# Performance work log

Measured on AMD Instinct MI355X. Metric: run time of the kernel, lower is better.

Reference implementation:

```python
import jax, jax.numpy as jnp
import numpy as np

B, J, D = 1024, 17, 512          # batch, joints, encoder hidden dim
M, K, DT = 34, 2048, 512         # tokens per pose, codebook size, token dim
DDEC, DDEC_I = 32, 64            # decoder hidden dims
L_ENC, L_DEC = 4, 1
DECAY = 0.9
EPS = 1e-5


def _ln(x, g, b):
    m = jnp.mean(x, -1, keepdims=True)
    v = jnp.mean((x - m) ** 2, -1, keepdims=True)
    return (x - m) * jax.lax.rsqrt(v + EPS) * g + b


def _mlp(x, w1, b1, w2, b2):
    return jax.nn.gelu(x @ w1 + b1, approximate=False) @ w2 + b2


def _mixer(x, p, i):
    ln1g, ln1b, tw1, tb1, tw2, tb2, ln2g, ln2b, cw1, cb1, cw2, cb2 = (a[i] for a in p)
    y = jnp.swapaxes(_ln(x, ln1g, ln1b), 1, 2)        # token-mixing over joints
    y = jnp.swapaxes(_mlp(y, tw1, tb1, tw2, tb2), 1, 2)
    z = _mlp(_ln(x + y, ln2g, ln2b), cw1, cb1, cw2, cb2)  # channel-mixing
    return x + y + z


def _forward(joints, invisible_token, start_w, start_b,
             enc_ln1_g, enc_ln1_b, enc_tw1, enc_tb1, enc_tw2, enc_tb2,
             enc_ln2_g, enc_ln2_b, enc_cw1, enc_cb1, enc_cw2, enc_cb2,
             enc_ln_g, enc_ln_b, token_mlp_w, token_mlp_b, feat_w, feat_b,
             dec_ln1_g, dec_ln1_b, dec_tw1, dec_tb1, dec_tw2, dec_tb2,
             dec_ln2_g, dec_ln2_b, dec_cw1, dec_cb1, dec_cw2, dec_cb2,
             dec_token_mlp_w, dec_token_mlp_b, dec_start_w, dec_start_b,
             dec_ln_g, dec_ln_b, rec_w, rec_b,
             codebook, ema_cluster_size, ema_w):
    x = joints[:, :, :2] @ start_w + start_b                  # [B,J,D]
    vis = (joints[:, :, 2:] != 0).astype(x.dtype)             # [B,J,1]
    x = x * vis + invisible_token * (1.0 - vis)
    encp = (enc_ln1_g, enc_ln1_b, enc_tw1, enc_tb1, enc_tw2, enc_tb2,
            enc_ln2_g, enc_ln2_b, enc_cw1, enc_cb1, enc_cw2, enc_cb2)
    for i in range(L_ENC):
        x = _mixer(x, encp, i)
    x = _ln(x, enc_ln_g, enc_ln_b)
    # token_mlp: Linear over joints axis: [B,D,J] -> [B,D,M] -> [B,M,D]
    x = jnp.einsum('bjd,jm->bmd', x, token_mlp_w) + token_mlp_b[None, :, None]
    feat = (x @ feat_w + feat_b).reshape(B * M, DT)           # encode_feat [N,DT]
    # squared euclidean distances to codebook entries
    dists = (jnp.sum(feat * feat, 1, keepdims=True)
             + jnp.sum(codebook * codebook, 1)
             - 2.0 * feat @ codebook.T)                       # [N,K]
    idx = jnp.argmin(dists, axis=1)                           # [N]
    quant = codebook[idx]                                     # == one_hot(idx) @ codebook
    # EMA codebook update (buffers; single-device so all_reduce == identity)
    sg_feat = jax.lax.stop_gradient(feat)
    counts = jax.ops.segment_sum(jnp.ones((B * M,), feat.dtype), idx, num_segments=K)
    dw = jax.ops.segment_sum(sg_feat, idx, num_segments=K)    # == encodings.T @ feat
    cs = ema_cluster_size * DECAY + (1.0 - DECAY) * counts
    n = jnp.sum(cs)
    cs = (cs + 1e-5) / (n + K * 1e-5) * n                     # laplace smoothing
    ema_w_new = ema_w * DECAY + (1.0 - DECAY) * dw
    codebook_new = ema_w_new / cs[:, None]
    e_latent_loss = jnp.mean(jnp.square(jax.lax.stop_gradient(quant) - feat))
    quant = feat + jax.lax.stop_gradient(quant - feat)        # straight-through
    ptf = quant.reshape(B, M, DT)
    out_ptf = jax.lax.stop_gradient(ptf)
    # decoder_token_mlp: Linear over token axis: [B,DT,M] -> [B,DT,J] -> [B,J,DT]
    y = jnp.einsum('bmd,mj->bjd', ptf, dec_token_mlp_w) + dec_token_mlp_b[None, :, None]
    y = y @ dec_start_w + dec_start_b                         # [B,J,DDEC]
    decp = (dec_ln1_g, dec_ln1_b, dec_tw1, dec_tb1, dec_tw2, dec_tb2,
            dec_ln2_g, dec_ln2_b, dec_cw1, dec_cb1, dec_cw2, dec_cb2)
    for i in range(L_DEC):
        y = _mixer(y, decp, i)
    y = _ln(y, dec_ln_g, dec_ln_b)
    rec = y @ rec_w + rec_b                                   # [B,J,2]
    return rec, idx, e_latent_loss, out_ptf, codebook_new


def setup_inputs():
    ks = iter(jax.random.split(jax.random.key(0), 64))
    def nrm(shape, s=0.02):
        return jax.random.normal(next(ks), shape, jnp.float32) * s
    inp = {}
    coords = jax.random.uniform(next(ks), (B, J, 2), jnp.float32)
    inp['joints'] = jnp.concatenate([coords, jnp.ones((B, J, 1), jnp.float32)], -1)
    inp['joints_feature'] = nrm((B, J, 256), 1.0)   # unused (guide_ratio=0)
    inp['cls_logits'] = jnp.zeros((1, 1), jnp.float32)  # unused in tokenizer stage
    inp['invisible_token'] = nrm((1, 1, D))
    inp['start_w'], inp['start_b'] = nrm((2, D)), jnp.zeros((D,), jnp.float32)
    for pre, L, H, HI in (('enc', L_ENC, D, D), ('dec', L_DEC, DDEC, DDEC_I)):
        inp[pre + '_ln1_g'], inp[pre + '_ln1_b'] = jnp.ones((L, H)), jnp.zeros((L, H))
        inp[pre + '_tw1'], inp[pre + '_tb1'] = nrm((L, J, 64)), jnp.zeros((L, 64))
        inp[pre + '_tw2'], inp[pre + '_tb2'] = nrm((L, 64, J)), jnp.zeros((L, J))
        inp[pre + '_ln2_g'], inp[pre + '_ln2_b'] = jnp.ones((L, H)), jnp.zeros((L, H))
        inp[pre + '_cw1'], inp[pre + '_cb1'] = nrm((L, H, HI)), jnp.zeros((L, HI))
        inp[pre + '_cw2'], inp[pre + '_cb2'] = nrm((L, HI, H)), jnp.zeros((L, H))
    inp['enc_ln_g'], inp['enc_ln_b'] = jnp.ones((D,)), jnp.zeros((D,))
    inp['token_mlp_w'], inp['token_mlp_b'] = nrm((J, M)), jnp.zeros((M,))
    inp['feat_w'], inp['feat_b'] = nrm((D, DT)), jnp.zeros((DT,))
    inp['codebook'] = jax.random.normal(next(ks), (K, DT), jnp.float32)
    inp['ema_cluster_size'] = jnp.zeros((K,), jnp.float32)
    inp['ema_w'] = jax.random.normal(next(ks), (K, DT), jnp.float32)
    inp['dec_token_mlp_w'], inp['dec_token_mlp_b'] = nrm((M, J)), jnp.zeros((J,))
    inp['dec_start_w'], inp['dec_start_b'] = nrm((DT, DDEC)), jnp.zeros((DDEC,))
    inp['dec_ln_g'], inp['dec_ln_b'] = jnp.ones((DDEC,)), jnp.zeros((DDEC,))
    inp['rec_w'], inp['rec_b'] = nrm((DDEC, 2)), jnp.zeros((2,))
    return inp


def reference(joints, joints_feature, cls_logits, invisible_token, start_w, start_b,
              enc_ln1_g, enc_ln1_b, enc_tw1, enc_tb1, enc_tw2, enc_tb2,
              enc_ln2_g, enc_ln2_b, enc_cw1, enc_cb1, enc_cw2, enc_cb2,
              enc_ln_g, enc_ln_b, token_mlp_w, token_mlp_b, feat_w, feat_b,
              codebook, ema_cluster_size, ema_w,
              dec_ln1_g, dec_ln1_b, dec_tw1, dec_tb1, dec_tw2, dec_tb2,
              dec_ln2_g, dec_ln2_b, dec_cw1, dec_cb1, dec_cw2, dec_cb2,
              dec_token_mlp_w, dec_token_mlp_b, dec_start_w, dec_start_b,
              dec_ln_g, dec_ln_b, rec_w, rec_b):
    # joints_feature / cls_logits unused: guide_ratio=0, stage_pct='tokenizer'
    return _forward(joints, invisible_token, start_w, start_b,
                    enc_ln1_g, enc_ln1_b, enc_tw1, enc_tb1, enc_tw2, enc_tb2,
                    enc_ln2_g, enc_ln2_b, enc_cw1, enc_cb1, enc_cw2, enc_cb2,
                    enc_ln_g, enc_ln_b, token_mlp_w, token_mlp_b, feat_w, feat_b,
                    dec_ln1_g, dec_ln1_b, dec_tw1, dec_tb1, dec_tw2, dec_tb2,
                    dec_ln2_g, dec_ln2_b, dec_cw1, dec_cb1, dec_cw2, dec_cb2,
                    dec_token_mlp_w, dec_token_mlp_b, dec_start_w, dec_start_b,
                    dec_ln_g, dec_ln_b, rec_w, rec_b,
                    codebook, ema_cluster_size, ema_w)
```

## Files before the change

kernel.cpp:

```cpp
#include <hip/hip_runtime.h>
#include <math.h>

constexpr int Bn = 1024, Jn = 17, Mn = 34;
constexpr int RJ = Bn * Jn;
constexpr int RM = Bn * Mn;
constexpr size_t SZX = (size_t)RJ * 512;
constexpr size_t SZM = (size_t)RM * 512;

typedef __attribute__((ext_vector_type(8))) short bf16x8;
typedef __attribute__((ext_vector_type(4))) float f32x4;
typedef unsigned long long u64;
typedef unsigned short u16;
typedef unsigned int u32;

__device__ __forceinline__ float gelu_f(float x) {
  return 0.5f * x * (1.0f + erff(x * 0.7071067811865475f));
}
__device__ __forceinline__ u16 bf16_rne(float x) {
  u32 u = __float_as_uint(x);
  u += 0x7fffu + ((u >> 16) & 1u);
  return (u16)(u >> 16);
}
__device__ __forceinline__ float bf16_f(u16 h) {
  return __uint_as_float((u32)h << 16);
}

typedef __attribute__((address_space(1))) const void gas_t;
typedef __attribute__((address_space(3))) void las_t;
__device__ __forceinline__ void gll16(const void* g, void* l) {
  __builtin_amdgcn_global_load_lds((gas_t*)g, (las_t*)l, 16, 0, 0);
}

__global__ __launch_bounds__(256) void embed_kernel(
    const float* __restrict__ joints, const float* __restrict__ inv,
    const float* __restrict__ sw, const float* __restrict__ sb,
    float* __restrict__ out) {
  int tid = blockIdx.x * 256 + threadIdx.x;
  int row = tid >> 9, d = tid & 511;
  float j0 = joints[row * 3 + 0];
  float j1 = joints[row * 3 + 1];
  float j2 = joints[row * 3 + 2];
  float x = fmaf(j0, sw[d], fmaf(j1, sw[512 + d], sb[d]));
  float v = (j2 != 0.0f) ? 1.0f : 0.0f;
  out[tid] = x * v + inv[d] * (1.0f - v);
}

__global__ __launch_bounds__(256) void mixer_fused(
    const float* __restrict__ x_in, float* __restrict__ res_out,
    u16* __restrict__ oh, u16* __restrict__ ol,
    const float* __restrict__ g1, const float* __restrict__ b1,
    const float* __restrict__ tw1, const float* __restrict__ tb1,
    const float* __restrict__ tw2, const float* __restrict__ tb2,
    const float* __restrict__ g2, const float* __restrict__ b2) {
  __shared__ float xs[17][512];
  __shared__ float sw1[17 * 64], sw2[64 * 17], sb1v[64], sb2v[17];
  __shared__ float stats[17][2];
  const int tid = threadIdx.x;
  const int b = blockIdx.x;
  for (int i = tid; i < 17 * 64; i += 256) { sw1[i] = tw1[i]; sw2[i] = tw2[i]; }
  if (tid < 64) sb1v[tid] = tb1[tid];
  if (tid < 17) sb2v[tid] = tb2[tid];
  const float* px = x_in + (size_t)b * 17 * 512;
  for (int i = tid; i < 17 * 512; i += 256) xs[i >> 9][i & 511] = px[i];
  __syncthreads();
  const int wv = tid >> 6, ln_ = tid & 63;
  for (int j = wv; j < 17; j += 4) {
    float v[8];
    float s = 0.0f;
#pragma unroll
    for (int i = 0; i < 8; i++) { v[i] = xs[j][ln_ + 64 * i]; s += v[i]; }
#pragma unroll
    for (int m = 32; m; m >>= 1) s += __shfl_xor(s, m);
    float mean = s * (1.0f / 512.0f);
    float s2 = 0.0f;
#pragma unroll
    for (int i = 0; i < 8; i++) { float t = v[i] - mean; s2 += t * t; }
#pragma unroll
    for (int m = 32; m; m >>= 1) s2 += __shfl_xor(s2, m);
    float rs = 1.0f / sqrtf(s2 * (1.0f / 512.0f) + 1e-5f);
    if (ln_ == 0) { stats[j][0] = mean; stats[j][1] = rs; }
  }
  __syncthreads();
  for (int cc = 0; cc < 2; cc++) {
    int d = tid + cc * 256;
    float gd = g1[d], bd = b1[d];
    float t[17], acc[17];
#pragma unroll
    for (int j = 0; j < 17; j++) {
      t[j] = (xs[j][d] - stats[j][0]) * stats[j][1] * gd + bd;
      acc[j] = 0.0f;
    }
    for (int k = 0; k < 64; k++) {
      float h = sb1v[k];
#pragma unroll
      for (int j = 0; j < 17; j++) h = fmaf(t[j], sw1[j * 64 + k], h);
      h = gelu_f(h);
#pragma unroll
      for (int j = 0; j < 17; j++) acc[j] = fmaf(h, sw2[k * 17 + j], acc[j]);
    }
#pragma unroll
    for (int j = 0; j < 17; j++) {
      float r = xs[j][d] + acc[j] + sb2v[j];
      xs[j][d] = r;
      res_out[((size_t)b * 17 + j) * 512 + d] = r;
    }
  }
  __syncthreads();
  for (int j = wv; j < 17; j += 4) {
    float v[8];
    float s = 0.0f;
#pragma unroll
    for (int i = 0; i < 8; i++) { v[i] = xs[j][ln_ + 64 * i]; s += v[i]; }
#pragma unroll
    for (int m = 32; m; m >>= 1) s += __shfl_xor(s, m);
    float mean = s * (1.0f / 512.0f);
    float s2 = 0.0f;
#pragma unroll
    for (int i = 0; i < 8; i++) { float t = v[i] - mean; s2 += t * t; }
#pragma unroll
    for (int m = 32; m; m >>= 1) s2 += __shfl_xor(s2, m);
    float rs = 1.0f / sqrtf(s2 * (1.0f / 512.0f) + 1e-5f);
#pragma unroll
    for (int i = 0; i < 8; i++) {
      int d = ln_ + 64 * i;
      float o = (v[i] - mean) * rs * g2[d] + b2[d];
      u16 h = bf16_rne(o);
      size_t off = ((size_t)b * 17 + j) * 512 + d;
      oh[off] = h;
      ol[off] = bf16_rne(o - bf16_f(h));
    }
  }
}

__global__ __launch_bounds__(256) void lnmix_fused(
    const float* __restrict__ x_in, u16* __restrict__ oh, u16* __restrict__ ol,
    const float* __restrict__ g, const float* __restrict__ bb,
    const float* __restrict__ w, const float* __restrict__ bias) {
  __shared__ float xs[17][513];
  __shared__ float sw[17 * 34], sb[34];
  const int tid = threadIdx.x;
  const int b = blockIdx.x;
  for (int i = tid; i < 17 * 34; i += 256) sw[i] = w[i];
  if (tid < 34) sb[tid] = bias[tid];
  const float* px = x_in + (size_t)b * 17 * 512;
  for (int i = tid; i < 17 * 512; i += 256) xs[i >> 9][i & 511] = px[i];
  __syncthreads();
  const int wv = tid >> 6, ln_ = tid & 63;
  for (int j = wv; j < 17; j += 4) {
    float v[8];
    float s = 0.0f;
#pragma unroll
    for (int i = 0; i < 8; i++) { v[i] = xs[j][ln_ + 64 * i]; s += v[i]; }
#pragma unroll
    for (int m = 32; m; m >>= 1) s += __shfl_xor(s, m);
    float mean = s * (1.0f / 512.0f);
    float s2 = 0.0f;
#pragma unroll
    for (int i = 0; i < 8; i++) { float t = v[i] - mean; s2 += t * t; }
#pragma unroll
    for (int m = 32; m; m >>= 1) s2 += __shfl_xor(s2, m);
    float rs = 1.0f / sqrtf(s2 * (1.0f / 512.0f) + 1e-5f);
#pragma unroll
    for (int i = 0; i < 8; i++) {
      int d = ln_ + 64 * i;
      xs[j][d] = (v[i] - mean) * rs * g[d] + bb[d];
    }
  }
  __syncthreads();
  for (int cc = 0; cc < 2; cc++) {
    int d = tid + cc * 256;
    float t[17];
#pragma unroll
    for (int j = 0; j < 17; j++) t[j] = xs[j][d];
#pragma unroll
    for (int m = 0; m < 34; m++) {
      float s = sb[m];
#pragma unroll
      for (int j = 0; j < 17; j++) s = fmaf(t[j], sw[j * 34 + m], s);
      size_t o = ((size_t)b * 34 + m) * 512 + d;
      u16 h = bf16_rne(s);
      oh[o] = h;
      ol[o] = bf16_rne(s - bf16_f(h));
    }
  }
}

__global__ __launch_bounds__(256) void prep2_wT(
    const float* __restrict__ W1, const float* __restrict__ W2,
    u16* __restrict__ Th1, u16* __restrict__ Tl1,
    u16* __restrict__ Th2, u16* __restrict__ Tl2) {
  int tid = blockIdx.x * 256 + threadIdx.x;
  const float* W = (tid < 262144) ? W1 : W2;
  u16* Th = (tid < 262144) ? Th1 : Th2;
  u16* Tl = (tid < 262144) ? Tl1 : Tl2;
  int t = tid & 262143;
  int k = t >> 9, n = t & 511;
  float v = W[t];
  u16 h = bf16_rne(v);
  Th[(size_t)n * 512 + k] = h;
  Tl[(size_t)n * 512 + k] = bf16_rne(v - bf16_f(h));
}

__global__ __launch_bounds__(256) void prep_wT(
    const float* __restrict__ W, u16* __restrict__ Th, u16* __restrict__ Tl) {
  int tid = blockIdx.x * 256 + threadIdx.x;
  int k = tid >> 9, n = tid & 511;
  float v = W[tid];
  u16 h = bf16_rne(v);
  Th[(size_t)n * 512 + k] = h;
  Tl[(size_t)n * 512 + k] = bf16_rne(v - bf16_f(h));
}

__global__ __launch_bounds__(256) void splitnorm_kernel(
    const float* __restrict__ CBm, u16* __restrict__ hi, u16* __restrict__ lo,
    float* __restrict__ cnorm) {
  int wave = threadIdx.x >> 6, lane = threadIdx.x & 63;
  int k = blockIdx.x * 4 + wave;
  const float4* p4 = (const float4*)(CBm + (size_t)k * 512);
  ushort4* h4 = (ushort4*)(hi + (size_t)k * 512);
  ushort4* l4 = (ushort4*)(lo + (size_t)k * 512);
  float s = 0.0f;
#pragma unroll
  for (int i = 0; i < 2; i++) {
    float4 x = p4[lane + 64 * i];
    ushort4 h, l;
    h.x = bf16_rne(x.x); l.x = bf16_rne(x.x - bf16_f(h.x));
    h.y = bf16_rne(x.y); l.y = bf16_rne(x.y - bf16_f(h.y));
    h.z = bf16_rne(x.z); l.z = bf16_rne(x.z - bf16_f(h.z));
    h.w = bf16_rne(x.w); l.w = bf16_rne(x.w - bf16_f(h.w));
    h4[lane + 64 * i] = h;
    l4[lane + 64 * i] = l;
    s = fmaf(x.x, x.x, s); s = fmaf(x.y, x.y, s);
    s = fmaf(x.z, x.z, s); s = fmaf(x.w, x.w, s);
  }
#pragma unroll
  for (int m = 32; m; m >>= 1) s += __shfl_xor(s, m);
  if (lane == 0) cnorm[k] = s;
}

#define MG_PROLOGUE()                                                        \
  const int tid = threadIdx.x;                                               \
  const int m0 = blockIdx.x * 128, n0 = blockIdx.y * 128;                    \
  const int lane = tid & 63, wave = tid >> 6;                                \
  const int wm = wave >> 1, wn = wave & 1;                                   \
  const int fr = lane & 15, q = lane >> 4, qd = q;                           \
  const int ci0 = wave * 128 + lane, ci1 = ci0 + 64;                         \
  const int r0 = ci0 >> 2, c0x = (ci0 & 3) ^ ((r0 >> 1) & 3);                \
  const int r1 = ci1 >> 2, c1x = (ci1 & 3) ^ ((r1 >> 1) & 3);                \
  const size_t aoff0 = (size_t)(m0 + r0) * 512 + c0x * 8;                    \
  const size_t aoff1 = (size_t)(m0 + r1) * 512 + c1x * 8;                    \
  const size_t boff0 = (size_t)(n0 + r0) * 512 + c0x * 8;                    \
  const size_t boff1 = (size_t)(n0 + r1) * 512 + c1x * 8;                    \
  const int ld0 = wave * 1024, ld1 = ld0 + 512;       \
  int fca[4], fcb[4];                                                        \
  _Pragma("unroll") for (int t4 = 0; t4 < 4; t4++) {                         \
    int rra = wm * 64 + t4 * 16 + fr;                                        \
    int rrb = wn * 64 + t4 * 16 + fr;                                        \
    int sz = q ^ ((fr >> 1) & 3);                                            \
    fca[t4] = (rra * 4 + sz) * 8;                                            \
    fcb[t4] = (rrb * 4 + sz) * 8;                                            \
  }                                                                          \
  f32x4 acc[4][4];                                                           \
  _Pragma("unroll") for (int i = 0; i < 4; i++)                              \
    _Pragma("unroll") for (int j = 0; j < 4; j++) {                          \
      acc[i][j][0] = 0.0f; acc[i][j][1] = 0.0f;                              \
      acc[i][j][2] = 0.0f; acc[i][j][3] = 0.0f;                              \
    }

#define MG_KLOOP(Ah, Al, Bh, Bl)                                             \
  for (int k0 = 0; k0 < 512; k0 += 32) {                                     \
    gll16(Ah + aoff0 + k0, &sAh[ld0]);                                       \
    gll16(Ah + aoff1 + k0, &sAh[ld1]);                                       \
    gll16(Al + aoff0 + k0, &sAl[ld0]);                                       \
    gll16(Al + aoff1 + k0, &sAl[ld1]);                                       \
    gll16(Bh + boff0 + k0, &sBh[ld0]);                                       \
    gll16(Bh + boff1 + k0, &sBh[ld1]);                                       \
    gll16(Bl + boff0 + k0, &sBl[ld0]);                                       \
    gll16(Bl + boff1 + k0, &sBl[ld1]);                                       \
    __syncthreads();                                                         \
    bf16x8 fah[4], fal[4], fbh[4], fbl[4];                                   \
    _Pragma("unroll") for (int t4 = 0; t4 < 4; t4++) {                       \
      fah[t4] = *(const bf16x8*)&sAh[fca[t4]];                               \
      fal[t4] = *(const bf16x8*)&sAl[fca[t4]];                               \
      fbh[t4] = *(const bf16x8*)&sBh[fcb[t4]];                               \
      fbl[t4] = *(const bf16x8*)&sBl[fcb[t4]];                               \
    }                                                                        \
    _Pragma("unroll") for (int mt = 0; mt < 4; mt++)                         \
      _Pragma("unroll") for (int nt = 0; nt < 4; nt++) {                     \
        acc[mt][nt] = __builtin_amdgcn_mfma_f32_16x16x32_bf16(               \
            fah[mt], fbh[nt], acc[mt][nt], 0, 0, 0);                         \
        acc[mt][nt] = __builtin_amdgcn_mfma_f32_16x16x32_bf16(               \
            fah[mt], fbl[nt], acc[mt][nt], 0, 0, 0);                         \
        acc[mt][nt] = __builtin_amdgcn_mfma_f32_16x16x32_bf16(               \
            fal[mt], fbh[nt], acc[mt][nt], 0, 0, 0);                         \
      }                                                                      \
    __syncthreads();                                                         \
  }

template <int GELU_FLAG, int RES_FLAG, int HILO_OUT>
__global__ __launch_bounds__(256, 4) void mgemm(
    const u16* __restrict__ Ah, const u16* __restrict__ Al,
    const u16* __restrict__ Bh, const u16* __restrict__ Bl,
    const float* __restrict__ bias, const float* __restrict__ R,
    float* __restrict__ C, u16* __restrict__ Oh, u16* __restrict__ Ol, int N) {
  __shared__ __align__(16) u16 sAh[4096], sAl[4096], sBh[4096], sBl[4096];
  MG_PROLOGUE()
  MG_KLOOP(Ah, Al, Bh, Bl)
#pragma unroll
  for (int mt = 0; mt < 4; mt++)
#pragma unroll
    for (int reg = 0; reg < 4; reg++) {
      int row = m0 + wm * 64 + mt * 16 + qd * 4 + reg;
#pragma unroll
      for (int nt = 0; nt < 4; nt++) {
        int col = n0 + wn * 64 + nt * 16 + fr;
        float v = acc[mt][nt][reg] + bias[col];
        if (GELU_FLAG) v = gelu_f(v);
        if (RES_FLAG) v += R[(size_t)row * N + col];
        if (HILO_OUT) {
          u16 h = bf16_rne(v);
          Oh[(size_t)row * N + col] = h;
          Ol[(size_t)row * N + col] = bf16_rne(v - bf16_f(h));
        } else {
          C[(size_t)row * N + col] = v;
        }
      }
    }
}

__global__ __launch_bounds__(256, 4) void dist_mfma(
    const u16* __restrict__ Ah, const u16* __restrict__ Al,
    const u16* __restrict__ Bh, const u16* __restrict__ Bl,
    const float* __restrict__ cnorm, u64* __restrict__ packed) {
  __shared__ __align__(16) u16 sAh[4096], sAl[4096], sBh[4096], sBl[4096];
  MG_PROLOGUE()
  MG_KLOOP(Ah, Al, Bh, Bl)
#pragma unroll
  for (int mt = 0; mt < 4; mt++)
#pragma unroll
    for (int reg = 0; reg < 4; reg++) {
      u64 best = ~0ull;
#pragma unroll
      for (int nt = 0; nt < 4; nt++) {
        int c = n0 + wn * 64 + nt * 16 + fr;
        float d = cnorm[c] - 2.0f * acc[mt][nt][reg];
        u32 ub = __float_as_uint(d);
        ub = (ub & 0x80000000u) ? ~ub : (ub | 0x80000000u);
        u64 p = ((u64)ub << 32) | (u32)c;
        best = (p < best) ? p : best;
      }
#pragma unroll
      for (int mm = 1; mm <= 8; mm <<= 1) {
        u32 h2 = __shfl_xor((u32)(best >> 32), mm);
        u32 l2 = __shfl_xor((u32)best, mm);
        u64 o = ((u64)h2 << 32) | l2;
        best = (o < best) ? o : best;
      }
      if (fr == 0) {
        int row = m0 + wm * 64 + mt * 16 + qd * 4 + reg;
        atomicMin(&packed[row], best);
      }
    }
}

__global__ __launch_bounds__(256) void idxcount_kernel(
    const u64* __restrict__ packed, float* __restrict__ o_idx,
    int* __restrict__ cnt) {
  __shared__ int h[2048];
  for (int i = threadIdx.x; i < 2048; i += 256) h[i] = 0;
  __syncthreads();
  int r = blockIdx.x * 256 + threadIdx.x;
  u32 k = (u32)packed[r];
  o_idx[r] = (float)k;
  atomicAdd(&h[k], 1);
  __syncthreads();
  for (int i = threadIdx.x; i < 2048; i += 256) {
    int v = h[i];
    if (v) atomicAdd(&cnt[i], v);
  }
}

__global__ __launch_bounds__(256) void scan_kernel(
    const int* __restrict__ cnt, int* __restrict__ base,
    int* __restrict__ cursor, const float* __restrict__ ema_cs,
    float* __restrict__ nbuf) {
  __shared__ int part[256];
  __shared__ float esum[256];
  int t = threadIdx.x;
  int local[8];
  int s = 0;
  float es = 0.0f;
#pragma unroll
  for (int i = 0; i < 8; i++) {
    local[i] = cnt[t * 8 + i];
    s += local[i];
    es += ema_cs[t * 8 + i];
  }
  part[t] = s;
  esum[t] = es;
  __syncthreads();
  for (int off = 1; off < 256; off <<= 1) {
    int v = (t >= off) ? part[t - off] : 0;
    __syncthreads();
    part[t] += v;
    __syncthreads();
  }
  int run = part[t] - s;
#pragma unroll
  for (int i = 0; i < 8; i++) {
    base[t * 8 + i] = run;
    cursor[t * 8 + i] = run;
    run += local[i];
  }
  for (int o = 128; o; o >>= 1) {
    if (t < o) esum[t] += esum[t + o];
    __syncthreads();
  }
  if (t == 0) nbuf[0] = 0.9f * esum[0] + 0.1f * (float)RM;
}

__global__ __launch_bounds__(256) void scatter_kernel(
    const u64* __restrict__ packed, int* __restrict__ cursor,
    u32* __restrict__ bucket) {
  __shared__ int h[2048];
  __shared__ int gb[2048];
  for (int i = threadIdx.x; i < 2048; i += 256) h[i] = 0;
  __syncthreads();
  int r = blockIdx.x * 256 + threadIdx.x;
  int k = (int)(u32)packed[r];
  int lrank = atomicAdd(&h[k], 1);
  __syncthreads();
  for (int i = threadIdx.x; i < 2048; i += 256) {
    int v = h[i];
    gb[i] = v ? atomicAdd(&cursor[i], v) : 0;
  }
  __syncthreads();
  bucket[gb[k] + lrank] = ((u32)k << 17) | (u32)r;
}

__global__ __launch_bounds__(256) void quant_out_kernel(
    const u16* __restrict__ fh, const u16* __restrict__ fl,
    const float* __restrict__ CBm, const u64* __restrict__ packed,
    float* __restrict__ ptf_out, float* __restrict__ lpart) {
  __shared__ float wred[4];
  int row = blockIdx.x * 2 + (threadIdx.x >> 7);
  int t = threadIdx.x & 127;
  int k = (int)(u32)packed[row];
  uint2 hb = ((const uint2*)(fh + (size_t)row * 512))[t];
  uint2 lb = ((const uint2*)(fl + (size_t)row * 512))[t];
  float f0 = bf16_f((u16)hb.x) + bf16_f((u16)lb.x);
  float f1 = bf16_f((u16)(hb.x >> 16)) + bf16_f((u16)(lb.x >> 16));
  float f2 = bf16_f((u16)hb.y) + bf16_f((u16)lb.y);
  float f3 = bf16_f((u16)(hb.y >> 16)) + bf16_f((u16)(lb.y >> 16));
  float4 c = ((const float4*)(CBm + (size_t)k * 512))[t];
  float* po = ptf_out + (size_t)row * 512 + 4 * t;
  po[0] = c.x; po[1] = c.y; po[2] = c.z; po[3] = c.w;
  float dx = c.x - f0, dy = c.y - f1, dz = c.z - f2, dwv = c.w - f3;
  float ls = dx * dx + dy * dy + dz * dz + dwv * dwv;
#pragma unroll
  for (int m = 32; m; m >>= 1) ls += __shfl_xor(ls, m);
  if ((threadIdx.x & 63) == 0) wred[threadIdx.x >> 6] = ls;
  __syncthreads();
  if (threadIdx.x == 0)
    lpart[blockIdx.x] = wred[0] + wred[1] + wred[2] + wred[3];
}

__global__ __launch_bounds__(256) void loss_final_kernel(
    const float* __restrict__ lpart, float* __restrict__ loss_out) {
  __shared__ float red[256];
  float s = 0.0f;
  for (int i = threadIdx.x; i < RM / 2; i += 256) s += lpart[i];
  red[threadIdx.x] = s;
  __syncthreads();
  for (int o = 128; o; o >>= 1) {
    if (threadIdx.x < o) red[threadIdx.x] += red[threadIdx.x + o];
    __syncthreads();
  }
  if (threadIdx.x == 0)
    loss_out[0] = red[0] / (float)((size_t)RM * 512);
}

__global__ __launch_bounds__(256) void dwsum_chunk_kernel(
    const u16* __restrict__ fh, const u16* __restrict__ fl,
    const u32* __restrict__ bucket, float* __restrict__ dw) {
  __shared__ u32 sp[64];
  const int t = threadIdx.x;
  if (t < 64) sp[t] = bucket[blockIdx.x * 64 + t];
  __syncthreads();
  float ax = 0.0f, ay = 0.0f;
  int curk = (int)(sp[0] >> 17);
  u32 hb = *(const u32*)(fh + (size_t)(sp[0] & 0x1FFFF) * 512 + 2 * t);
  u32 lb = *(const u32*)(fl + (size_t)(sp[0] & 0x1FFFF) * 512 + 2 * t);
  for (int i = 0; i < 64; i++) {
    u32 hn = 0, ln2 = 0;
    if (i + 1 < 64) {
      hn = *(const u32*)(fh + (size_t)(sp[i + 1] & 0x1FFFF) * 512 + 2 * t);
      ln2 = *(const u32*)(fl + (size_t)(sp[i + 1] & 0x1FFFF) * 512 + 2 * t);
    }
    int k = (int)(sp[i] >> 17);
    if (k != curk) {
      atomicAdd(&dw[(size_t)curk * 512 + 2 * t], ax);
      atomicAdd(&dw[(size_t)curk * 512 + 2 * t + 1], ay);
      ax = 0.0f; ay = 0.0f; curk = k;
    }
    ax += bf16_f((u16)hb) + bf16_f((u16)lb);
    ay += bf16_f((u16)(hb >> 16)) + bf16_f((u16)(lb >> 16));
    hb = hn; lb = ln2;
  }
  atomicAdd(&dw[(size_t)curk * 512 + 2 * t], ax);
  atomicAdd(&dw[(size_t)curk * 512 + 2 * t + 1], ay);
}

__global__ __launch_bounds__(256) void cbnew_kernel(
    const float* __restrict__ ema_w, const float* __restrict__ dw,
    const float* __restrict__ ema_cs, const int* __restrict__ cnt,
    const float* __restrict__ nbuf, float* __restrict__ outp) {
  int tid = blockIdx.x * 256 + threadIdx.x;
  int k = tid >> 9;
  float n = nbuf[0];
  float cs = ema_cs[k] * 0.9f + 0.1f * (float)cnt[k];
  cs = (cs + 1e-5f) / (n + 0.02048f) * n;
  outp[tid] = (ema_w[tid] * 0.9f + 0.1f * dw[tid]) / cs;
}

__global__ __launch_bounds__(256) void decoder_fused(
    const float* __restrict__ ptf,
    const float* __restrict__ dtokw, const float* __restrict__ dtokb,
    const float* __restrict__ dsw, const float* __restrict__ dsb,
    const float* __restrict__ ln1g, const float* __restrict__ ln1b,
    const float* __restrict__ tw1, const float* __restrict__ tb1,
    const float* __restrict__ tw2, const float* __restrict__ tb2,
    const float* __restrict__ ln2g, const float* __restrict__ ln2b,
    const float* __restrict__ cw1, const float* __restrict__ cb1,
    const float* __restrict__ cw2, const float* __restrict__ cb2,
    const float* __restrict__ lng, const float* __restrict__ lnb,
    const float* __restrict__ recw, const float* __restrict__ recb,
    float* __restrict__ o_rec) {
  __shared__ float buf[34 * 257];
  __shared__ float yS[17][257];
  __shared__ float zS[17][33];
  __shared__ float t2S[17][33];
  __shared__ float hS[17][65];
  __shared__ float sdw[34 * 17];
  __shared__ float stw1[17 * 64], stw2[64 * 17];
  const int tid = threadIdx.x;
  const int b = blockIdx.x;
  for (int i = tid; i < 34 * 17; i += 256) sdw[i] = dtokw[i];
  for (int i = tid; i < 17 * 64; i += 256) { stw1[i] = tw1[i]; stw2[i] = tw2[i]; }
  float zacc0 = 0.0f, zacc1 = 0.0f, zacc2 = 0.0f;
  const int j0 = tid >> 5, dd0 = tid & 31;
  const int p1 = tid + 256;
  const int j1 = p1 >> 5, dd1 = p1 & 31;
  const int p2 = tid + 512;
  const int j2 = p2 >> 5, dd2 = p2 & 31;
  for (int ch = 0; ch < 2; ch++) {
    for (int m = 0; m < 34; m++)
      buf[m * 257 + tid] = ptf[((size_t)b * 34 + m) * 512 + ch * 256 + tid];
    __syncthreads();
#pragma unroll 1
    for (int j = 0; j < 17; j++) {
      float s = dtokb[j];
#pragma unroll
      for (int m = 0; m < 34; m++) s = fmaf(buf[m * 257 + tid], sdw[m * 17 + j], s);
      yS[j][tid] = s;
    }
    __syncthreads();
    for (int i = tid; i < 256 * 32; i += 256) {
      int d = i >> 5, dd = i & 31;
      buf[d * 33 + dd] = dsw[(size_t)(ch * 256 + d) * 32 + dd];
    }
    __syncthreads();
    {
      float s = 0.0f;
      for (int d = 0; d < 256; d++) s = fmaf(yS[j0][d], buf[d * 33 + dd0], s);
      zacc0 += s;
      float s1 = 0.0f;
      for (int d = 0; d < 256; d++) s1 = fmaf(yS[j1][d], buf[d * 33 + dd1], s1);
      zacc1 += s1;
      if (tid < 32) {
        float s2 = 0.0f;
        for (int d = 0; d < 256; d++) s2 = fmaf(yS[j2][d], buf[d * 33 + dd2], s2);
        zacc2 += s2;
      }
    }
    __syncthreads();
  }
  zS[j0][dd0] = zacc0 + dsb[dd0];
  zS[j1][dd1] = zacc1 + dsb[dd1];
  if (tid < 32) zS[j2][dd2] = zacc2 + dsb[dd2];
  __syncthreads();
  if (tid < 17) {
    float m = 0.0f;
#pragma unroll
    for (int d = 0; d < 32; d++) m += zS[tid][d];
    m *= (1.0f / 32.0f);
    float v = 0.0f;
#pragma unroll
    for (int d = 0; d < 32; d++) { float t = zS[tid][d] - m; v += t * t; }
    float rs = 1.0f / sqrtf(v * (1.0f / 32.0f) + 1e-5f);
#pragma unroll
    for (int d = 0; d < 32; d++)
      t2S[tid][d] = (zS[tid][d] - m) * rs * ln1g[d] + ln1b[d];
  }
  __syncthreads();
  if (tid < 32) {
    float t[17], acc[17];
#pragma unroll
    for (int j = 0; j < 17; j++) { t[j] = t2S[j][tid]; acc[j] = 0.0f; }
    for (int k = 0; k < 64; k++) {
      float h = tb1[k];
#pragma unroll
      for (int j = 0; j < 17; j++) h = fmaf(t[j], stw1[j * 64 + k], h);
      h = gelu_f(h);
#pragma unroll
      for (int j = 0; j < 17; j++) acc[j] = fmaf(h, stw2[k * 17 + j], acc[j]);
    }
#pragma unroll
    for (int j = 0; j < 17; j++) zS[j][tid] = zS[j][tid] + acc[j] + tb2[j];
  }
  __syncthreads();
  if (tid < 17) {
    float m = 0.0f;
#pragma unroll
    for (int d = 0; d < 32; d++) m += zS[tid][d];
    m *= (1.0f / 32.0f);
    float v = 0.0f;
#pragma unroll
    for (int d = 0; d < 32; d++) { float t = zS[tid][d] - m; v += t * t; }
    float rs = 1.0f / sqrtf(v * (1.0f / 32.0f) + 1e-5f);
#pragma unroll
    for (int d = 0; d < 32; d++)
      t2S[tid][d] = (zS[tid][d] - m) * rs * ln2g[d] + ln2b[d];
  }
  __syncthreads();
  for (int p = tid; p < 17 * 64; p += 256) {
    int j = p >> 6, k = p & 63;
    float s = cb1[k];
#pragma unroll
    for (int d = 0; d < 32; d++) s = fmaf(t2S[j][d], cw1[d * 64 + k], s);
    hS[j][k] = gelu_f(s);
  }
  __syncthreads();
  {
    float s = cb2[dd0];
#pragma unroll
    for (int k = 0; k < 64; k++) s = fmaf(hS[j0][k], cw2[k * 32 + dd0], s);
    zS[j0][dd0] += s;
    float s1 = cb2[dd1];
#pragma unroll
    for (int k = 0; k < 64; k++) s1 = fmaf(hS[j1][k], cw2[k * 32 + dd1], s1);
    zS[j1][dd1] += s1;
    if (tid < 32) {
      float s2 = cb2[dd2];
#pragma unroll
      for (int k = 0; k < 64; k++) s2 = fmaf(hS[j2][k], cw2[k * 32 + dd2], s2);
      zS[j2][dd2] += s2;
    }
  }
  __syncthreads();
  if (tid < 17) {
    float m = 0.0f;
#pragma unroll
    for (int d = 0; d < 32; d++) m += zS[tid][d];
    m *= (1.0f / 32.0f);
    float v = 0.0f;
#pragma unroll
    for (int d = 0; d < 32; d++) { float t = zS[tid][d] - m; v += t * t; }
    float rs = 1.0f / sqrtf(v * (1.0f / 32.0f) + 1e-5f);
#pragma unroll
    for (int d = 0; d < 32; d++)
      t2S[tid][d] = (zS[tid][d] - m) * rs * lng[d] + lnb[d];
  }
  __syncthreads();
  if (tid < 34) {
    int j = tid >> 1, c = tid & 1;
    float s = recb[c];
#pragma unroll
    for (int d = 0; d < 32; d++) s = fmaf(t2S[j][d], recw[d * 2 + c], s);
    o_rec[((size_t)b * 17 + j) * 2 + c] = s;
  }
}

extern "C" void kernel_launch(void* const* d_in, const int* in_sizes, int n_in,
                              void* d_out, int out_size, void* d_ws, size_t ws_size,
                              hipStream_t stream) {
  const float* joints   = (const float*)d_in[0];
  const float* inv_tok  = (const float*)d_in[3];
  const float* start_w  = (const float*)d_in[4];
  const float* start_b  = (const float*)d_in[5];
  const float* e_ln1g = (const float*)d_in[6];
  const float* e_ln1b = (const float*)d_in[7];
  const float* e_tw1  = (const float*)d_in[8];
  const float* e_tb1  = (const float*)d_in[9];
  const float* e_tw2  = (const float*)d_in[10];
  const float* e_tb2  = (const float*)d_in[11];
  const float* e_ln2g = (const float*)d_in[12];
  const float* e_ln2b = (const float*)d_in[13];
  const float* e_cw1  = (const float*)d_in[14];
  const float* e_cb1  = (const float*)d_in[15];
  const float* e_cw2  = (const float*)d_in[16];
  const float* e_cb2  = (const float*)d_in[17];
  const float* d_ln1g = (const float*)d_in[18];
  const float* d_ln1b = (const float*)d_in[19];
  const float* d_tw1  = (const float*)d_in[20];
  const float* d_tb1  = (const float*)d_in[21];
  const float* d_tw2  = (const float*)d_in[22];
  const float* d_tb2  = (const float*)d_in[23];
  const float* d_ln2g = (const float*)d_in[24];
  const float* d_ln2b = (const float*)d_in[25];
  const float* d_cw1  = (const float*)d_in[26];
  const float* d_cb1  = (const float*)d_in[27];
  const float* d_cw2  = (const float*)d_in[28];
  const float* d_cb2  = (const float*)d_in[29];
  const float* enc_lng = (const float*)d_in[30];
  const float* enc_lnb = (const float*)d_in[31];
  const float* tok_w   = (const float*)d_in[32];
  const float* tok_b   = (const float*)d_in[33];
  const float* feat_w  = (const float*)d_in[34];
  const float* feat_b  = (const float*)d_in[35];
  const float* codebook = (const float*)d_in[36];
  const float* ema_cs   = (const float*)d_in[37];
  const float* ema_w    = (const float*)d_in[38];
  const float* dtok_w   = (const float*)d_in[39];
  const float* dtok_b   = (const float*)d_in[40];
  const float* dstart_w = (const float*)d_in[41];
  const float* dstart_b = (const float*)d_in[42];
  const float* dec_lng  = (const float*)d_in[43];
  const float* dec_lnb  = (const float*)d_in[44];
  const float* rec_w    = (const float*)d_in[45];
  const float* rec_b    = (const float*)d_in[46];

  float* ws = (float*)d_ws;
  float* Ab  = ws;
  float* Bb  = ws + SZX;
  float* Cc  = ws + 2 * SZX;
  float* P1e = ws + 3 * SZX;
  float* P2e = ws + 4 * SZX;
  float* cbs = ws + 5 * SZX;
  float* cnorm = cbs + 1048576;
  u64*  packed = (u64*)(cnorm + 2048);
  int*  cnt    = (int*)(cnorm + 2048 + 69632);
  int*  basebuf = cnt + 2048;
  int*  cursor  = basebuf + 2048;
  u32*  bucket  = (u32*)(cursor + 2048);
  float* lpart  = (float*)(bucket + RM);
  float* nbuf   = lpart + RM / 2;
  float* dw     = nbuf + 2048;
  u16* WTh1 = (u16*)dw;
  u16* WTl1 = (u16*)(dw + 131072);
  u16* WTh2 = (u16*)(dw + 262144);
  u16* WTl2 = (u16*)(dw + 393216);
  u16* P1eh = (u16*)P1e;  u16* P1el = (u16*)(P1e + SZX / 2);
  u16* P2eh = (u16*)P2e;  u16* P2el = (u16*)(P2e + SZX / 2);
  u16* P1mh = (u16*)Ab;   u16* P1ml = (u16*)Bb;
  u16* P2mh = (u16*)Cc;   u16* P2ml = (u16*)P1e;
  u16* chh = (u16*)cbs;   u16* cll = (u16*)(cbs + 524288);

  float* outp = (float*)d_out;
  float* o_rec = outp;
  float* o_idx = outp + (size_t)RJ * 2;
  float* o_loss = o_idx + RM;
  float* o_ptf = o_loss + 1;
  float* o_cb = o_ptf + SZM;

  embed_kernel<<<(RJ * 512) / 256, 256, 0, stream>>>(joints, inv_tok, start_w, start_b, Ab);
  for (int i = 0; i < 4; i++) {
    prep2_wT<<<2048, 256, 0, stream>>>(
        e_cw1 + (size_t)i * 512 * 512, e_cw2 + (size_t)i * 512 * 512,
        WTh1, WTl1, WTh2, WTl2);
    mixer_fused<<<Bn, 256, 0, stream>>>(
        Ab, Bb, P1eh, P1el,
        e_ln1g + i * 512, e_ln1b + i * 512,
        e_tw1 + i * 17 * 64, e_tb1 + i * 64, e_tw2 + i * 64 * 17, e_tb2 + i * 17,
        e_ln2g + i * 512, e_ln2b + i * 512);
    mgemm<1, 0, 1><<<dim3(RJ / 128, 4), 256, 0, stream>>>(
        P1eh, P1el, WTh1, WTl1, e_cb1 + i * 512, nullptr, nullptr, P2eh, P2el, 512);
    mgemm<0, 1, 0><<<dim3(RJ / 128, 4), 256, 0, stream>>>(
        P2eh, P2el, WTh2, WTl2, e_cb2 + i * 512, Bb, Ab, nullptr, nullptr, 512);
  }
  lnmix_fused<<<Bn, 256, 0, stream>>>(Ab, P1mh, P1ml, enc_lng, enc_lnb, tok_w, tok_b);
  prep_wT<<<1024, 256, 0, stream>>>(feat_w, WTh1, WTl1);
  mgemm<0, 0, 1><<<dim3(RM / 128, 4), 256, 0, stream>>>(
      P1mh, P1ml, WTh1, WTl1, feat_b, nullptr, nullptr, P2mh, P2ml, 512);

  splitnorm_kernel<<<2048 / 4, 256, 0, stream>>>(codebook, chh, cll, cnorm);
  hipMemsetAsync(packed, 0xFF, (size_t)RM * 8, stream);
  dist_mfma<<<dim3(RM / 128, 2048 / 128), 256, 0, stream>>>(P2mh, P2ml, chh, cll, cnorm, packed);

  hipMemsetAsync(cnt, 0, 2048 * sizeof(int), stream);
  idxcount_kernel<<<RM / 256, 256, 0, stream>>>(packed, o_idx, cnt);
  scan_kernel<<<1, 256, 0, stream>>>(cnt, basebuf, cursor, ema_cs, nbuf);
  scatter_kernel<<<RM / 256, 256, 0, stream>>>(packed, cursor, bucket);
  quant_out_kernel<<<RM / 2, 256, 0, stream>>>(P2mh, P2ml, codebook, packed, o_ptf, lpart);
  loss_final_kernel<<<1, 256, 0, stream>>>(lpart, o_loss);
  hipMemsetAsync(dw, 0, (size_t)2048 * 512 * sizeof(float), stream);
  dwsum_chunk_kernel<<<RM / 64, 256, 0, stream>>>(P2mh, P2ml, bucket, dw);
  cbnew_kernel<<<(2048 * 512) / 256, 256, 0, stream>>>(ema_w, dw, ema_cs, cnt, nbuf, o_cb);

  decoder_fused<<<Bn, 256, 0, stream>>>(
      o_ptf, dtok_w, dtok_b, dstart_w, dstart_b,
      d_ln1g, d_ln1b, d_tw1, d_tb1, d_tw2, d_tb2, d_ln2g, d_ln2b,
      d_cw1, d_cb1, d_cw2, d_cb2, dec_lng, dec_lnb, rec_w, rec_b, o_rec);
}
```

Measured before the change: 1.627 ms.

## Fold weight prep, memsets and loss reduction into neighbor kernels; use 64-row GEMM tiles

Weight transpose/split work moves into mixer_fused and lnmix_fused, and the separate prep kernels are removed. The memsets of packed, cnt and dw are folded into splitnorm and scatter, and the loss final reduction moves into cbnew block 0. The channel-mixing GEMMs switch to a 64x128 tile with double the block count. The aim is fewer launches and better GEMM occupancy, at the cost of less B-tile reuse and a serial reduction inside one cbnew block.

After: 1.616 ms. Within noise of the previous version (-0.7%).

```diff
diff --git a/kernel.cpp b/kernel.cpp
--- a/kernel.cpp
+++ b/kernel.cpp
@@ -51,12 +51,27 @@
     const float* __restrict__ g1, const float* __restrict__ b1,
     const float* __restrict__ tw1, const float* __restrict__ tb1,
     const float* __restrict__ tw2, const float* __restrict__ tb2,
-    const float* __restrict__ g2, const float* __restrict__ b2) {
+    const float* __restrict__ g2, const float* __restrict__ b2,
+    const float* __restrict__ W1, const float* __restrict__ W2,
+    u16* __restrict__ Th1, u16* __restrict__ Tl1,
+    u16* __restrict__ Th2, u16* __restrict__ Tl2) {
   __shared__ float xs[17][512];
   __shared__ float sw1[17 * 64], sw2[64 * 17], sb1v[64], sb2v[17];
   __shared__ float stats[17][2];
   const int tid = threadIdx.x;
   const int b = blockIdx.x;
+  {
+    int gid = b * 256 + tid;
+    int k = gid >> 9, n = gid & 511;
+    float v = W1[gid];
+    u16 h = bf16_rne(v);
+    Th1[(size_t)n * 512 + k] = h;
+    Tl1[(size_t)n * 512 + k] = bf16_rne(v - bf16_f(h));
+    v = W2[gid];
+    h = bf16_rne(v);
+    Th2[(size_t)n * 512 + k] = h;
+    Tl2[(size_t)n * 512 + k] = bf16_rne(v - bf16_f(h));
+  }
   for (int i = tid; i < 17 * 64; i += 256) { sw1[i] = tw1[i]; sw2[i] = tw2[i]; }
   if (tid < 64) sb1v[tid] = tb1[tid];
   if (tid < 17) sb2v[tid] = tb2[tid];
@@ -135,11 +150,20 @@
 __global__ __launch_bounds__(256) void lnmix_fused(
     const float* __restrict__ x_in, u16* __restrict__ oh, u16* __restrict__ ol,
     const float* __restrict__ g, const float* __restrict__ bb,
-    const float* __restrict__ w, const float* __restrict__ bias) {
+    const float* __restrict__ w, const float* __restrict__ bias,
+    const float* __restrict__ Wf, u16* __restrict__ Thf, u16* __restrict__ Tlf) {
   __shared__ float xs[17][513];
   __shared__ float sw[17 * 34], sb[34];
   const int tid = threadIdx.x;
   const int b = blockIdx.x;
+  {
+    int gid = b * 256 + tid;
+    int k = gid >> 9, n = gid & 511;
+    float v = Wf[gid];
+    u16 h = bf16_rne(v);
+    Thf[(size_t)n * 512 + k] = h;
+    Tlf[(size_t)n * 512 + k] = bf16_rne(v - bf16_f(h));
+  }
   for (int i = tid; i < 17 * 34; i += 256) sw[i] = w[i];
   if (tid < 34) sb[tid] = bias[tid];
   const float* px = x_in + (size_t)b * 17 * 512;
@@ -185,35 +209,12 @@
   }
 }
 
-__global__ __launch_bounds__(256) void prep2_wT(
-    const float* __restrict__ W1, const float* __restrict__ W2,
-    u16* __restrict__ Th1, u16* __restrict__ Tl1,
-    u16* __restrict__ Th2, u16* __restrict__ Tl2) {
-  int tid = blockIdx.x * 256 + threadIdx.x;
-  const float* W = (tid < 262144) ? W1 : W2;
-  u16* Th = (tid < 262144) ? Th1 : Th2;
-  u16* Tl = (tid < 262144) ? Tl1 : Tl2;
-  int t = tid & 262143;
-  int k = t >> 9, n = t & 511;
-  float v = W[t];
-  u16 h = bf16_rne(v);
-  Th[(size_t)n * 512 + k] = h;
-  Tl[(size_t)n * 512 + k] = bf16_rne(v - bf16_f(h));
-}
-
-__global__ __launch_bounds__(256) void prep_wT(
-    const float* __restrict__ W, u16* __restrict__ Th, u16* __restrict__ Tl) {
-  int tid = blockIdx.x * 256 + threadIdx.x;
-  int k = tid >> 9, n = tid & 511;
-  float v = W[tid];
-  u16 h = bf16_rne(v);
-  Th[(size_t)n * 512 + k] = h;
-  Tl[(size_t)n * 512 + k] = bf16_rne(v - bf16_f(h));
-}
-
 __global__ __launch_bounds__(256) void splitnorm_kernel(
     const float* __restrict__ CBm, u16* __restrict__ hi, u16* __restrict__ lo,
-    float* __restrict__ cnorm) {
+    float* __restrict__ cnorm, u64* __restrict__ packed, int* __restrict__ cnt) {
+  int gid = blockIdx.x * 256 + threadIdx.x;
+  for (int i = gid; i < RM; i += 131072) packed[i] = ~0ull;
+  if (gid < 2048) cnt[gid] = 0;
   int wave = threadIdx.x >> 6, lane = threadIdx.x & 63;
   int k = blockIdx.x * 4 + wave;
   const float4* p4 = (const float4*)(CBm + (size_t)k * 512);
@@ -236,6 +237,100 @@
 #pragma unroll
   for (int m = 32; m; m >>= 1) s += __shfl_xor(s, m);
   if (lane == 0) cnorm[k] = s;
+}
+
+template <int GELU_FLAG, int RES_FLAG, int HILO_OUT>
+__global__ __launch_bounds__(256, 4) void mgemm64(
+    const u16* __restrict__ Ah, const u16* __restrict__ Al,
+    const u16* __restrict__ Bh, const u16* __restrict__ Bl,
+    const float* __restrict__ bias, const float* __restrict__ R,
+    float* __restrict__ C, u16* __restrict__ Oh, u16* __restrict__ Ol, int N) {
+  __shared__ __align__(16) u16 sAh[2048], sAl[2048], sBh[4096], sBl[4096];
+  const int tid = threadIdx.x;
+  const int m0 = blockIdx.x * 64, n0 = blockIdx.y * 128;
+  const int lane = tid & 63, wave = tid >> 6;
+  const int wm = wave >> 1, wn = wave & 1;
+  const int fr = lane & 15, q = lane >> 4;
+  const int ra = tid >> 2, ca = (tid & 3) ^ ((ra >> 1) & 3);
+  const size_t aoff = (size_t)(m0 + ra) * 512 + ca * 8;
+  const int rb0 = tid >> 2, cb0 = (tid & 3) ^ ((rb0 >> 1) & 3);
+  const int ci1 = tid + 256;
+  const int rb1 = ci1 >> 2, cb1 = (ci1 & 3) ^ ((rb1 >> 1) & 3);
+  const size_t boff0 = (size_t)(n0 + rb0) * 512 + cb0 * 8;
+  const size_t boff1 = (size_t)(n0 + rb1) * 512 + cb1 * 8;
+  const int ldA = wave * 512;
+  const int ldB0 = wave * 512, ldB1 = 2048 + wave * 512;
+  int fca[2], fcb[4];
+#pragma unroll
+  for (int mt = 0; mt < 2; mt++) {
+    int rra = wm * 32 + mt * 16 + fr;
+    fca[mt] = (rra * 4 + (q ^ ((rra >> 1) & 3))) * 8;
+  }
+#pragma unroll
+  for (int nt = 0; nt < 4; nt++) {
+    int rrb = wn * 64 + nt * 16 + fr;
+    fcb[nt] = (rrb * 4 + (q ^ ((rrb >> 1) & 3))) * 8;
+  }
+  f32x4 acc[2][4];
+#pragma unroll
+  for (int i = 0; i < 2; i++)
+#pragma unroll
+    for (int j = 0; j < 4; j++) {
+      acc[i][j][0] = 0.0f; acc[i][j][1] = 0.0f;
+      acc[i][j][2] = 0.0f; acc[i][j][3] = 0.0f;
+    }
+  for (int k0 = 0; k0 < 512; k0 += 32) {
+    gll16(Ah + aoff + k0, &sAh[ldA]);
+    gll16(Al + aoff + k0, &sAl[ldA]);
+    gll16(Bh + boff0 + k0, &sBh[ldB0]);
+    gll16(Bh + boff1 + k0, &sBh[ldB1]);
+    gll16(Bl + boff0 + k0, &sBl[ldB0]);
+    gll16(Bl + boff1 + k0, &sBl[ldB1]);
+    __syncthreads();
+    bf16x8 fah[2], fal[2], fbh[4], fbl[4];
+#pragma unroll
+    for (int mt = 0; mt < 2; mt++) {
+      fah[mt] = *(const bf16x8*)&sAh[fca[mt]];
+      fal[mt] = *(const bf16x8*)&sAl[fca[mt]];
+    }
+#pragma unroll
+    for (int nt = 0; nt < 4; nt++) {
+      fbh[nt] = *(const bf16x8*)&sBh[fcb[nt]];
+      fbl[nt] = *(const bf16x8*)&sBl[fcb[nt]];
+    }
+#pragma unroll
+    for (int mt = 0; mt < 2; mt++)
+#pragma unroll
+      for (int nt = 0; nt < 4; nt++) {
+        acc[mt][nt] = __builtin_amdgcn_mfma_f32_16x16x32_bf16(
+            fah[mt], fbh[nt], acc[mt][nt], 0, 0, 0);
+        acc[mt][nt] = __builtin_amdgcn_mfma_f32_16x16x32_bf16(
+            fah[mt], fbl[nt], acc[mt][nt], 0, 0, 0);
+        acc[mt][nt] = __builtin_amdgcn_mfma_f32_16x16x32_bf16(
+            fal[mt], fbh[nt], acc[mt][nt], 0, 0, 0);
+      }
+    __syncthreads();
+  }
+#pragma unroll
+  for (int mt = 0; mt < 2; mt++)
+#pragma unroll
+    for (int reg = 0; reg < 4; reg++) {
+      int row = m0 + wm * 32 + mt * 16 + q * 4 + reg;
+#pragma unroll
+      for (int nt = 0; nt < 4; nt++) {
+        int col = n0 + wn * 64 + nt * 16 + fr;
+        float v = acc[mt][nt][reg] + bias[col];
+        if (GELU_FLAG) v = gelu_f(v);
+        if (RES_FLAG) v += R[(size_t)row * N + col];
+        if (HILO_OUT) {
+          u16 h = bf16_rne(v);
+          Oh[(size_t)row * N + col] = h;
+          Ol[(size_t)row * N + col] = bf16_rne(v - bf16_f(h));
+        } else {
+          C[(size_t)row * N + col] = v;
+        }
+      }
+    }
 }
 
 #define MG_PROLOGUE()                                                        \
@@ -297,37 +392,6 @@
     __syncthreads();                                                         \
   }
 
-template <int GELU_FLAG, int RES_FLAG, int HILO_OUT>
-__global__ __launch_bounds__(256, 4) void mgemm(
-    const u16* __restrict__ Ah, const u16* __restrict__ Al,
-    const u16* __restrict__ Bh, const u16* __restrict__ Bl,
-    const float* __restrict__ bias, const float* __restrict__ R,
-    float* __restrict__ C, u16* __restrict__ Oh, u16* __restrict__ Ol, int N) {
-  __shared__ __align__(16) u16 sAh[4096], sAl[4096], sBh[4096], sBl[4096];
-  MG_PROLOGUE()
-  MG_KLOOP(Ah, Al, Bh, Bl)
-#pragma unroll
-  for (int mt = 0; mt < 4; mt++)
-#pragma unroll
-    for (int reg = 0; reg < 4; reg++) {
-      int row = m0 + wm * 64 + mt * 16 + qd * 4 + reg;
-#pragma unroll
-      for (int nt = 0; nt < 4; nt++) {
-        int col = n0 + wn * 64 + nt * 16 + fr;
-        float v = acc[mt][nt][reg] + bias[col];
-        if (GELU_FLAG) v = gelu_f(v);
-        if (RES_FLAG) v += R[(size_t)row * N + col];
-        if (HILO_OUT) {
-          u16 h = bf16_rne(v);
-          Oh[(size_t)row * N + col] = h;
-          Ol[(size_t)row * N + col] = bf16_rne(v - bf16_f(h));
-        } else {
-          C[(size_t)row * N + col] = v;
-        }
-      }
-    }
-}
-
 __global__ __launch_bounds__(256, 4) void dist_mfma(
     const u16* __restrict__ Ah, const u16* __restrict__ Al,
     const u16* __restrict__ Bh, const u16* __restrict__ Bl,
@@ -421,13 +485,14 @@
 
 __global__ __launch_bounds__(256) void scatter_kernel(
     const u64* __restrict__ packed, int* __restrict__ cursor,
-    u32* __restrict__ bucket) {
+    u32* __restrict__ bucket, float* __restrict__ dw) {
   __shared__ int h[2048];
   __shared__ int gb[2048];
+  int gid = blockIdx.x * 256 + threadIdx.x;
+  for (int i = gid; i < 2048 * 512; i += RM) dw[i] = 0.0f;
   for (int i = threadIdx.x; i < 2048; i += 256) h[i] = 0;
   __syncthreads();
-  int r = blockIdx.x * 256 + threadIdx.x;
-  int k = (int)(u32)packed[r];
+  int k = (int)(u32)packed[gid];
   int lrank = atomicAdd(&h[k], 1);
   __syncthreads();
   for (int i = threadIdx.x; i < 2048; i += 256) {
@@ -435,7 +500,7 @@
     gb[i] = v ? atomicAdd(&cursor[i], v) : 0;
   }
   __syncthreads();
-  bucket[gb[k] + lrank] = ((u32)k << 17) | (u32)r;
+  bucket[gb[k] + lrank] = ((u32)k << 17) | (u32)gid;
 }
 
 __global__ __launch_bounds__(256) void quant_out_kernel(
@@ -465,21 +530,6 @@
     lpart[blockIdx.x] = wred[0] + wred[1] + wred[2] + wred[3];
 }
 
-__global__ __launch_bounds__(256) void loss_final_kernel(
-    const float* __restrict__ lpart, float* __restrict__ loss_out) {
-  __shared__ float red[256];
-  float s = 0.0f;
-  for (int i = threadIdx.x; i < RM / 2; i += 256) s += lpart[i];
-  red[threadIdx.x] = s;
-  __syncthreads();
-  for (int o = 128; o; o >>= 1) {
-    if (threadIdx.x < o) red[threadIdx.x] += red[threadIdx.x + o];
-    __syncthreads();
-  }
-  if (threadIdx.x == 0)
-    loss_out[0] = red[0] / (float)((size_t)RM * 512);
-}
-
 __global__ __launch_bounds__(256) void dwsum_chunk_kernel(
     const u16* __restrict__ fh, const u16* __restrict__ fl,
     const u32* __restrict__ bucket, float* __restrict__ dw) {
@@ -514,13 +564,27 @@
 __global__ __launch_bounds__(256) void cbnew_kernel(
     const float* __restrict__ ema_w, const float* __restrict__ dw,
     const float* __restrict__ ema_cs, const int* __restrict__ cnt,
-    const float* __restrict__ nbuf, float* __restrict__ outp) {
+    const float* __restrict__ nbuf, float* __restrict__ outp,
+    const float* __restrict__ lpart, float* __restrict__ loss_out) {
   int tid = blockIdx.x * 256 + threadIdx.x;
   int k = tid >> 9;
   float n = nbuf[0];
   float cs = ema_cs[k] * 0.9f + 0.1f * (float)cnt[k];
   cs = (cs + 1e-5f) / (n + 0.02048f) * n;
   outp[tid] = (ema_w[tid] * 0.9f + 0.1f * dw[tid]) / cs;
+  if (blockIdx.x == 0) {
+    __shared__ float red[256];
+    float s = 0.0f;
+    for (int i = threadIdx.x; i < RM / 2; i += 256) s += lpart[i];
+    red[threadIdx.x] = s;
+    __syncthreads();
+    for (int o = 128; o; o >>= 1) {
+      if (threadIdx.x < o) red[threadIdx.x] += red[threadIdx.x + o];
+      __syncthreads();
+    }
+    if (threadIdx.x == 0)
+      loss_out[0] = red[0] / (float)((size_t)RM * 512);
+  }
 }
 
 __global__ __launch_bounds__(256) void decoder_fused(
@@ -765,37 +829,33 @@
 
   embed_kernel<<<(RJ * 512) / 256, 256, 0, stream>>>(joints, inv_tok, start_w, start_b, Ab);
   for (int i = 0; i < 4; i++) {
-    prep2_wT<<<2048, 256, 0, stream>>>(
-        e_cw1 + (size_t)i * 512 * 512, e_cw2 + (size_t)i * 512 * 512,
-        WTh1, WTl1, WTh2, WTl2);
     mixer_fused<<<Bn, 256, 0, stream>>>(
         Ab, Bb, P1eh, P1el,
         e_ln1g + i * 512, e_ln1b + i * 512,
         e_tw1 + i * 17 * 64, e_tb1 + i * 64, e_tw2 + i * 64 * 17, e_tb2 + i * 17,
-        e_ln2g + i * 512, e_ln2b + i * 512);
-    mgemm<1, 0, 1><<<dim3(RJ / 128, 4), 256, 0, stream>>>(
+        e_ln2g + i * 512, e_ln2b + i * 512,
+        e_cw1 + (size_t)i * 512 * 512, e_cw2 + (size_t)i * 512 * 512,
+        WTh1, WTl1, WTh2, WTl2);
+    mgemm64<1, 0, 1><<<dim3(RJ / 64, 4), 256, 0, stream>>>(
         P1eh, P1el, WTh1, WTl1, e_cb1 + i * 512, nullptr, nullptr, P2eh, P2el, 512);
-    mgemm<0, 1, 0><<<dim3(RJ / 128, 4), 256, 0, stream>>>(
+    mgemm64<0, 1, 0><<<dim3(RJ / 64, 4), 256, 0, stream>>>(
         P2eh, P2el, WTh2, WTl2, e_cb2 + i * 512, Bb, Ab, nullptr, nullptr, 512);
   }
-  lnmix_fused<<<Bn, 256, 0, stream>>>(Ab, P1mh, P1ml, enc_lng, enc_lnb, tok_w, tok_b);
-  prep_wT<<<1024, 256, 0, stream>>>(feat_w, WTh1, WTl1);
-  mgemm<0, 0, 1><<<dim3(RM / 128, 4), 256, 0, stream>>>(
+  lnmix_fused<<<Bn, 256, 0, stream>>>(Ab, P1mh, P1ml, enc_lng, enc_lnb, tok_w, tok_b,
+                                      feat_w, WTh1, WTl1);
+  mgemm64<0, 0, 1><<<dim3(RM / 64, 4), 256, 0, stream>>>(
       P1mh, P1ml, WTh1, WTl1, feat_b, nullptr, nullptr, P2mh, P2ml, 512);
 
-  splitnorm_kernel<<<2048 / 4, 256, 0, stream>>>(codebook, chh, cll, cnorm);
-  hipMemsetAsync(packed, 0xFF, (size_t)RM * 8, stream);
+  splitnorm_kernel<<<2048 / 4, 256, 0, stream>>>(codebook, chh, cll, cnorm, packed, cnt);
   dist_mfma<<<dim3(RM / 128, 2048 / 128), 256, 0, stream>>>(P2mh, P2ml, chh, cll, cnorm, packed);
 
-  hipMemsetAsync(cnt, 0, 2048 * sizeof(int), stream);
   idxcount_kernel<<<RM / 256, 256, 0, stream>>>(packed, o_idx, cnt);
   scan_kernel<<<1, 256, 0, stream>>>(cnt, basebuf, cursor, ema_cs, nbuf);
-  scatter_kernel<<<RM / 256, 256, 0, stream>>>(packed, cursor, bucket);
+  scatter_kernel<<<RM / 256, 256, 0, stream>>>(packed, cursor, bucket, dw);
   quant_out_kernel<<<RM / 2, 256, 0, stream>>>(P2mh, P2ml, codebook, packed, o_ptf, lpart);
-  loss_final_kernel<<<1, 256, 0, stream>>>(lpart, o_loss);
-  hipMemsetAsync(dw, 0, (size_t)2048 * 512 * sizeof(float), stream);
   dwsum_chunk_kernel<<<RM / 64, 256, 0, stream>>>(P2mh, P2ml, bucket, dw);
-  cbnew_kernel<<<(2048 * 512) / 256, 256, 0, stream>>>(ema_w, dw, ema_cs, cnt, nbuf, o_cb);
+  cbnew_kernel<<<(2048 * 512) / 256, 256, 0, stream>>>(
+      ema_w, dw, ema_cs, cnt, nbuf, o_cb, lpart, o_loss);
 
   decoder_fused<<<Bn, 256, 0, stream>>>(
       o_ptf, dtok_w, dtok_b, dstart_w, dstart_b,
```
